# Kernel tuning notes

Hardware: AMD Instinct MI355X
Metric: run time of the kernel (lower is better)

## Reference

```python
import jax, jax.numpy as jnp
import numpy as np
from jax.ops import segment_sum

D = 64
NUM_REL = 500
NUM_NODES = 100000
NUM_EDGES = 2000000
BATCH = 8


def _mlp(x, W1, b1, W2, b2):
    # torch nn.Sequential(Linear, ReLU, Linear); W stored as [in, out]
    return jnp.maximum(x @ W1 + b1, 0.0) @ W2 + b2


def setup_inputs() -> dict:
    key = jax.random.key(0)
    ks = jax.random.split(key, 12)
    edge_index = jax.random.randint(ks[0], (2, NUM_EDGES), 0, NUM_NODES)
    edge_type = jax.random.randint(ks[1], (NUM_EDGES,), 0, NUM_REL)
    h_index = jax.random.randint(ks[2], (BATCH,), 0, NUM_NODES)
    relation_representations = jax.random.normal(ks[3], (NUM_REL, D), dtype=jnp.float32)
    s = 0.1
    params = dict(
        Wi1=jax.random.normal(ks[4], (2 * D, D), dtype=jnp.float32) * s,
        bi1=jnp.zeros((D,), jnp.float32),
        Wi2=jax.random.normal(ks[5], (D, D), dtype=jnp.float32) * s,
        bi2=jnp.zeros((D,), jnp.float32),
        Wc1=jax.random.normal(ks[6], (2 * D, D), dtype=jnp.float32) * s,
        bc1=jnp.zeros((D,), jnp.float32),
        Wc2=jax.random.normal(ks[7], (D, D), dtype=jnp.float32) * s,
        bc2=jnp.zeros((D,), jnp.float32),
        strength=jnp.asarray(0.1, jnp.float32),
    )
    return dict(edge_index=edge_index, edge_type=edge_type, h_index=h_index,
                relation_representations=relation_representations,
                num_nodes=NUM_NODES, **params)


def reference(edge_index, edge_type, h_index, relation_representations,
              num_nodes, Wi1, bi1, Wi2, bi2, Wc1, bc1, Wc2, bc2, strength):
    N = num_nodes
    rel_emb = relation_representations            # [R, D]
    rel_ctx = rel_emb.mean(axis=0)                # [D] global relation context
    src, dst = edge_index[0], edge_index[1]
    edge_rel = rel_emb[edge_type]                 # [E, D]
    not_self = (src != dst)                       # self-loop edge counted once per entity
    w_dst = not_self.astype(edge_rel.dtype)

    # per-node mean of incident-edge relation embeddings (valid_rels mean)
    feat_sum = segment_sum(edge_rel, src, num_segments=N) \
             + segment_sum(edge_rel * w_dst[:, None], dst, num_segments=N)   # [N, D]
    ones = jnp.ones_like(w_dst)
    cnt = segment_sum(ones, src, num_segments=N) \
        + segment_sum(w_dst, dst, num_segments=N)                            # [N]
    has_edge = cnt > 0
    avg = jnp.where(has_edge[:, None], feat_sum / jnp.maximum(cnt, 1.0)[:, None],
                    rel_ctx[None, :])             # [N, D] entity_relation_avg

    # nodes with at least one non-self neighbor
    nbr_cnt = segment_sum(w_dst, src, num_segments=N) \
            + segment_sum(w_dst, dst, num_segments=N)
    has_neighbor = nbr_cnt > 0

    ctx_b = jnp.broadcast_to(rel_ctx[None, :], avg.shape)
    interaction = _mlp(jnp.concatenate([avg, ctx_b], axis=-1), Wi1, bi1, Wi2, bi2)
    context = _mlp(jnp.concatenate([avg, avg], axis=-1), Wc1, bc1, Wc2, bc2)
    context_feat = jnp.where(has_neighbor[:, None], context, interaction)

    alpha = jnp.clip(strength, 0.0, 0.3)
    final = (1.0 - alpha) * avg + alpha * context_feat
    node_feat = jnp.where(has_edge[:, None], final, rel_ctx[None, :])        # [N, D]

    # relevant entities = query entities + 1-hop neighbors; others stay zero
    h_mask = jnp.zeros((N,), jnp.int32).at[h_index].set(1)
    nbr = jnp.zeros((N,), jnp.int32)
    nbr = nbr.at[dst].max(h_mask[src]).at[src].max(h_mask[dst])
    relevant = (h_mask + nbr) > 0                                            # [N]

    per_node = jnp.where(relevant[:, None], node_feat, 0.0)                  # [N, D]
    B = h_index.shape[0]
    return jnp.broadcast_to(per_node[None], (B, N, per_node.shape[-1]))      # [B, N, D]
```

## Files before the change

kernel.cpp:

```cpp
#include <hip/hip_runtime.h>

#define DD 64

typedef float f4v __attribute__((ext_vector_type(4)));

#define PACK(n, t, w) ((((unsigned)(n)) << 10) | (((unsigned)(t)) << 1) | (unsigned)(w))

__global__ __launch_bounds__(256) void k_fill0(float* __restrict__ out, size_t total4) {
    size_t i = (size_t)blockIdx.x * blockDim.x + threadIdx.x;
    const size_t stride = (size_t)gridDim.x * blockDim.x;
    f4v z = (f4v)(0.f);
    for (; i < total4; i += stride)
        __builtin_nontemporal_store(z, (f4v*)(out + i * 4));
}

__global__ void k_zero(unsigned* __restrict__ bitmap, int NB, int* __restrict__ counters) {
    int i = blockIdx.x * blockDim.x + threadIdx.x;
    if (i < NB) bitmap[i] = 0u;
    if (i < 2) counters[i] = 0;
}

__global__ __launch_bounds__(512) void k_ctx(const float* __restrict__ rel, int R,
                                             const int* __restrict__ h_index, int B,
                                             float* __restrict__ ctx,
                                             unsigned* __restrict__ bitmap) {
    __shared__ float part[8][DD];
    int lane = threadIdx.x & 63;
    int w = threadIdx.x >> 6;
    float s0 = 0.f, s1 = 0.f;
    int r = w;
    for (; r + 16 <= R; r += 16) {
        s0 += rel[(size_t)r * DD + lane];
        s1 += rel[(size_t)(r + 8) * DD + lane];
    }
    for (; r < R; r += 8) s0 += rel[(size_t)r * DD + lane];
    part[w][lane] = s0 + s1;
    __syncthreads();
    int t = threadIdx.x;
    if (t < DD) {
        float tot = 0.f;
#pragma unroll
        for (int i = 0; i < 8; ++i) tot += part[i][t];
        ctx[t] = tot / (float)R;
    }
    if (t < B) {
        int n = h_index[t];
        atomicOr(bitmap + ((unsigned)n >> 5), 1u << (n & 31));
    }
}

__device__ __forceinline__ bool is_q(int v, const int* hq) {
    bool m = false;
#pragma unroll
    for (int b = 0; b < 8; ++b) m |= (v == hq[b]);
    return m;
}

__global__ __launch_bounds__(256) void k_mark(const int* __restrict__ src,
                                              const int* __restrict__ dst,
                                              const int* __restrict__ h_index, int B,
                                              unsigned* __restrict__ bitmap, int E) {
    int hq[8];
#pragma unroll
    for (int b = 0; b < 8; ++b) hq[b] = (b < B) ? h_index[b] : -1;
    const int nth = gridDim.x * blockDim.x;
    const int tid = blockIdx.x * blockDim.x + threadIdx.x;
    const int E16 = E & ~15;
#define MARK1(sv, dv)                                                        \
    do {                                                                     \
        if (is_q(sv, hq)) atomicOr(bitmap + ((unsigned)(dv) >> 5), 1u << ((dv) & 31)); \
        if (is_q(dv, hq)) atomicOr(bitmap + ((unsigned)(sv) >> 5), 1u << ((sv) & 31)); \
    } while (0)
    for (int base = tid * 16; base < E16; base += nth * 16) {
        int4 s[4], d[4];
#pragma unroll
        for (int u = 0; u < 4; ++u) s[u] = *(const int4*)(src + base + u * 4);
#pragma unroll
        for (int u = 0; u < 4; ++u) d[u] = *(const int4*)(dst + base + u * 4);
#pragma unroll
        for (int u = 0; u < 4; ++u) {
            MARK1(s[u].x, d[u].x);
            MARK1(s[u].y, d[u].y);
            MARK1(s[u].z, d[u].z);
            MARK1(s[u].w, d[u].w);
        }
    }
    for (int e = E16 + tid; e < E; e += nth) MARK1(src[e], dst[e]);
#undef MARK1
}

__global__ __launch_bounds__(256) void k_compact(const unsigned* __restrict__ bitmap, int NB,
                                                 int* __restrict__ rel_list,
                                                 int* __restrict__ counters) {
    int i = blockIdx.x * blockDim.x + threadIdx.x;
    int lane = threadIdx.x & 63;
    unsigned word = (i < NB) ? bitmap[i] : 0u;
    int c = __popc(word);
    int incl = c;
#pragma unroll
    for (int sh = 1; sh < 64; sh <<= 1) {
        int t = __shfl_up(incl, sh);
        if (lane >= sh) incl += t;
    }
    int total = __shfl(incl, 63);
    if (total == 0) return;
    int b0 = 0;
    if (lane == 0) b0 = atomicAdd(counters + 0, total);
    b0 = __shfl(b0, 0);
    int off = b0 + incl - c;
    while (word) {
        int bit = __ffs(word) - 1;
        word &= word - 1;
        rel_list[off++] = i * 32 + bit;
    }
}

__global__ __launch_bounds__(256) void k_scan(const int* __restrict__ src,
                                              const int* __restrict__ dst,
                                              const int* __restrict__ etype,
                                              const unsigned* __restrict__ bitmap, int NB,
                                              unsigned* __restrict__ rlist,
                                              int* __restrict__ counters, int E) {
    extern __shared__ unsigned bm[];
    for (int i = threadIdx.x; i < NB; i += blockDim.x) bm[i] = bitmap[i];
    __syncthreads();
#define CHK(id) ((bm[(unsigned)(id) >> 5] >> ((unsigned)(id) & 31)) & 1u)
    const int lane = threadIdx.x & 63;
    const int wid = (blockIdx.x * blockDim.x + threadIdx.x) >> 6;
    const int nw = (gridDim.x * blockDim.x) >> 6;
    const int E16 = E & ~15;
    const int CH = 64 * 16;
    for (int cb = wid * CH; cb < E16; cb += nw * CH) {
        int base = cb + lane * 16;
        bool act = (base < E16);
        int4 s[4], d[4];
        if (act) {
#pragma unroll
            for (int u = 0; u < 4; ++u) s[u] = *(const int4*)(src + base + u * 4);
#pragma unroll
            for (int u = 0; u < 4; ++u) d[u] = *(const int4*)(dst + base + u * 4);
        }
        unsigned ms = 0u, md = 0u;
        if (act) {
#define TST(sv, dv, idx)                                        \
            do {                                                \
                unsigned bs = CHK(sv), bd = CHK(dv);            \
                unsigned neq = ((sv) != (dv)) ? 1u : 0u;        \
                ms |= bs << (idx);                              \
                md |= (bd & neq) << (idx);                      \
            } while (0)
#pragma unroll
            for (int u = 0; u < 4; ++u) {
                TST(s[u].x, d[u].x, u * 4 + 0);
                TST(s[u].y, d[u].y, u * 4 + 1);
                TST(s[u].z, d[u].z, u * 4 + 2);
                TST(s[u].w, d[u].w, u * 4 + 3);
            }
#undef TST
        }
        int c = __popc(ms) + __popc(md);
        int incl = c;
#pragma unroll
        for (int sh = 1; sh < 64; sh <<= 1) {
            int t = __shfl_up(incl, sh);
            if (lane >= sh) incl += t;
        }
        int total = __shfl(incl, 63);
        if (total == 0) continue;
        int b0 = 0;
        if (lane == 0) b0 = atomicAdd(counters + 1, total);
        b0 = __shfl(b0, 0);
        unsigned off = (unsigned)(b0 + incl - c);
        if (c) {
#define EMIT(sv, dv, idx)                                                     \
            do {                                                              \
                unsigned bit = 1u << (idx);                                   \
                if ((ms | md) & bit) {                                        \
                    int t = etype[base + (idx)];                              \
                    if (ms & bit) rlist[off++] = PACK(sv, t, ((sv) != (dv)) ? 1 : 0); \
                    if (md & bit) rlist[off++] = PACK(dv, t, 1);              \
                }                                                             \
            } while (0)
#pragma unroll
            for (int u = 0; u < 4; ++u) {
                EMIT(s[u].x, d[u].x, u * 4 + 0);
                EMIT(s[u].y, d[u].y, u * 4 + 1);
                EMIT(s[u].z, d[u].z, u * 4 + 2);
                EMIT(s[u].w, d[u].w, u * 4 + 3);
            }
#undef EMIT
        }
    }
    const int tid = blockIdx.x * blockDim.x + threadIdx.x;
    const int nth = gridDim.x * blockDim.x;
    for (int e = E16 + tid; e < E; e += nth) {
        int sv = src[e], dv = dst[e];
        unsigned bs = CHK(sv), bd = CHK(dv);
        unsigned neq = (sv != dv) ? 1u : 0u;
        int k = (int)bs + (int)(bd & neq);
        if (k == 0) continue;
        int t = etype[e];
        int o = atomicAdd(counters + 1, k);
        if (bs) rlist[o++] = PACK(sv, t, neq);
        if (bd & neq) rlist[o] = PACK(dv, t, 1);
    }
#undef CHK
}

__device__ __forceinline__ void proc_rec(unsigned rv, bool valid, int n,
                                         const float* __restrict__ rel, int lane,
                                         float& fs, int& cnt, int& nb) {
    bool want = valid && ((int)(rv >> 10) == n);
    unsigned long long mk = __ballot(want);
    while (mk) {
        int l = __ffsll(mk) - 1;
        mk &= mk - 1;
        unsigned v = __shfl(rv, l);
        int t = (int)((v >> 1) & 0x1FFu);
        fs += rel[t * DD + lane];
        cnt += 1;
        nb += (int)(v & 1u);
    }
}

__global__ __launch_bounds__(256) void k_gather(
    const int* __restrict__ rel_list, const int* __restrict__ counters,
    const unsigned* __restrict__ rlist,
    const float* __restrict__ rel, const float* __restrict__ ctx,
    const float* __restrict__ Wi1, const float* __restrict__ bi1,
    const float* __restrict__ Wi2, const float* __restrict__ bi2,
    const float* __restrict__ Wc1, const float* __restrict__ bc1,
    const float* __restrict__ Wc2, const float* __restrict__ bc2,
    const float* __restrict__ strength, float* __restrict__ out, int N, int B) {
    __shared__ float part[4][DD];
    __shared__ int pc[4], pn[4];
    int lane = threadIdx.x & 63;
    int wv = threadIdx.x >> 6;
    int C = counters[0];
    int M = counters[1];
    float alpha = fminf(fmaxf(strength[0], 0.f), 0.3f);
    float ctxj = ctx[lane];
    int nchunk = (M + 255) / 256;
    size_t plane = (size_t)N * DD;
    for (int i = blockIdx.x; i < C; i += gridDim.x) {
        int n = rel_list[i];
        float fs = 0.f;
        int cnt = 0, nb = 0;
        for (int ch = wv; ch < nchunk; ch += 4) {
            int bbase = ch * 256 + lane * 4;
            uint4 r = *(const uint4*)(rlist + bbase);
            proc_rec(r.x, bbase + 0 < M, n, rel, lane, fs, cnt, nb);
            proc_rec(r.y, bbase + 1 < M, n, rel, lane, fs, cnt, nb);
            proc_rec(r.z, bbase + 2 < M, n, rel, lane, fs, cnt, nb);
            proc_rec(r.w, bbase + 3 < M, n, rel, lane, fs, cnt, nb);
        }
        part[wv][lane] = fs;
        if (lane == 0) { pc[wv] = cnt; pn[wv] = nb; }
        __syncthreads();
        if (wv == 0) {
            fs = part[0][lane] + part[1][lane] + part[2][lane] + part[3][lane];
            cnt = pc[0] + pc[1] + pc[2] + pc[3];
            nb = pn[0] + pn[1] + pn[2] + pn[3];
            float res;
            if (cnt == 0) {
                res = ctxj;
            } else {
                float avg = fs / (float)cnt;
                bool hasnbr = (nb > 0);
                const float* W1 = hasnbr ? Wc1 : Wi1;
                const float* b1 = hasnbr ? bc1 : bi1;
                const float* W2 = hasnbr ? Wc2 : Wi2;
                const float* b2 = hasnbr ? bc2 : bi2;
                float h1 = b1[lane];
#pragma unroll 4
                for (int k = 0; k < DD; ++k) {
                    float a_k = __shfl(avg, k);
                    float x2 = hasnbr ? a_k : __shfl(ctxj, k);
                    h1 += a_k * W1[k * DD + lane] + x2 * W1[(DD + k) * DD + lane];
                }
                h1 = fmaxf(h1, 0.f);
                float o = b2[lane];
#pragma unroll 4
                for (int k = 0; k < DD; ++k)
                    o += __shfl(h1, k) * W2[k * DD + lane];
                res = (1.f - alpha) * avg + alpha * o;
            }
            float* p = out + (size_t)n * DD + lane;
            for (int b = 0; b < B; ++b) p[(size_t)b * plane] = res;
        }
        __syncthreads();
    }
}

extern "C" void kernel_launch(void* const* d_in, const int* in_sizes, int n_in,
                              void* d_out, int out_size, void* d_ws, size_t ws_size,
                              hipStream_t stream) {
    const int*   edge_index = (const int*)d_in[0];
    const int*   edge_type  = (const int*)d_in[1];
    const int*   h_index    = (const int*)d_in[2];
    const float* rel_emb    = (const float*)d_in[3];
    const float* Wi1 = (const float*)d_in[5];
    const float* bi1 = (const float*)d_in[6];
    const float* Wi2 = (const float*)d_in[7];
    const float* bi2 = (const float*)d_in[8];
    const float* Wc1 = (const float*)d_in[9];
    const float* bc1 = (const float*)d_in[10];
    const float* Wc2 = (const float*)d_in[11];
    const float* bc2 = (const float*)d_in[12];
    const float* strength = (const float*)d_in[13];
    float* out = (float*)d_out;

    const int E = in_sizes[1];
    const int B = in_sizes[2];
    const int R = in_sizes[3] / DD;
    const int N = out_size / (B * DD);
    const int NB = (N + 31) / 32;
    const int* src = edge_index;
    const int* dst = edge_index + E;

    char* w = (char*)d_ws;
    size_t off = 0;
    auto carve = [&](size_t bytes) -> char* {
        char* p = w + off;
        off += (bytes + 255) & ~(size_t)255;
        return p;
    };
    float*    ctx      = (float*)carve(DD * sizeof(float));
    int*      counters = (int*)carve(2 * sizeof(int));
    unsigned* bitmap   = (unsigned*)carve((size_t)NB * sizeof(unsigned));
    int*      rel_list = (int*)carve((size_t)N * sizeof(int));
    unsigned* rlist    = (unsigned*)carve(((size_t)2 * E + 512) * sizeof(unsigned));
    (void)ws_size; (void)n_in;

    const int BLK = 256;
    int gB = (NB + BLK - 1) / BLK;
    const int gE = 512;
    size_t total4 = (size_t)out_size / 4;

    hipLaunchKernelGGL(k_fill0, dim3(2048), dim3(BLK), 0, stream, out, total4);

    hipLaunchKernelGGL(k_zero, dim3(gB), dim3(BLK), 0, stream, bitmap, NB, counters);
    hipLaunchKernelGGL(k_ctx, dim3(1), dim3(512), 0, stream,
                       rel_emb, R, h_index, B, ctx, bitmap);
    hipLaunchKernelGGL(k_mark, dim3(gE), dim3(BLK), 0, stream,
                       src, dst, h_index, B, bitmap, E);
    hipLaunchKernelGGL(k_compact, dim3(gB), dim3(BLK), 0, stream,
                       bitmap, NB, rel_list, counters);
    hipLaunchKernelGGL(k_scan, dim3(gE), dim3(BLK), (size_t)NB * sizeof(unsigned), stream,
                       src, dst, edge_type, bitmap, NB, rlist, counters, E);
    hipLaunchKernelGGL(k_gather, dim3(512), dim3(BLK), 0, stream,
                       rel_list, counters, rlist, rel_emb, ctx,
                       Wi1, bi1, Wi2, bi2, Wc1, bc1, Wc2, bc2, strength, out, N, B);
}
```

Measured before the change: 109.6 us.

## Fuse zero/fill/compact kernels into mark and scan passes, raise grid size

Bitmap and counter zeroing are merged into the single-block context kernel. The output zero-fill is split in half and appended to the mark and scan kernels, and bitmap compaction is folded into the start of the scan kernel. The grid grows from 512 to 2048 blocks so the fused kernels cover all bitmap words. This cuts launches from seven to four and lets the large output fill overlap with the edge passes. In exchange, zeroing the bitmap with a single block is serial, and the compaction correctness now depends on the grid covering NB.

```diff
diff --git a/kernel.cpp b/kernel.cpp
--- a/kernel.cpp
+++ b/kernel.cpp
@@ -5,28 +5,18 @@
 typedef float f4v __attribute__((ext_vector_type(4)));
 
 #define PACK(n, t, w) ((((unsigned)(n)) << 10) | (((unsigned)(t)) << 1) | (unsigned)(w))
-
-__global__ __launch_bounds__(256) void k_fill0(float* __restrict__ out, size_t total4) {
-    size_t i = (size_t)blockIdx.x * blockDim.x + threadIdx.x;
-    const size_t stride = (size_t)gridDim.x * blockDim.x;
-    f4v z = (f4v)(0.f);
-    for (; i < total4; i += stride)
-        __builtin_nontemporal_store(z, (f4v*)(out + i * 4));
-}
-
-__global__ void k_zero(unsigned* __restrict__ bitmap, int NB, int* __restrict__ counters) {
-    int i = blockIdx.x * blockDim.x + threadIdx.x;
-    if (i < NB) bitmap[i] = 0u;
-    if (i < 2) counters[i] = 0;
-}
 
 __global__ __launch_bounds__(512) void k_ctx(const float* __restrict__ rel, int R,
                                              const int* __restrict__ h_index, int B,
                                              float* __restrict__ ctx,
-                                             unsigned* __restrict__ bitmap) {
+                                             unsigned* __restrict__ bitmap, int NB,
+                                             int* __restrict__ counters) {
     __shared__ float part[8][DD];
-    int lane = threadIdx.x & 63;
-    int w = threadIdx.x >> 6;
+    int t = threadIdx.x;
+    for (int i = t; i < NB; i += 512) bitmap[i] = 0u;
+    if (t < 2) counters[t] = 0;
+    int lane = t & 63;
+    int w = t >> 6;
     float s0 = 0.f, s1 = 0.f;
     int r = w;
     for (; r + 16 <= R; r += 16) {
@@ -36,7 +26,6 @@
     for (; r < R; r += 8) s0 += rel[(size_t)r * DD + lane];
     part[w][lane] = s0 + s1;
     __syncthreads();
-    int t = threadIdx.x;
     if (t < DD) {
         float tot = 0.f;
 #pragma unroll
@@ -56,10 +45,11 @@
     return m;
 }
 
-__global__ __launch_bounds__(256) void k_mark(const int* __restrict__ src,
-                                              const int* __restrict__ dst,
-                                              const int* __restrict__ h_index, int B,
-                                              unsigned* __restrict__ bitmap, int E) {
+__global__ __launch_bounds__(256) void k_markfill(const int* __restrict__ src,
+                                                  const int* __restrict__ dst,
+                                                  const int* __restrict__ h_index, int B,
+                                                  unsigned* __restrict__ bitmap, int E,
+                                                  float* __restrict__ out, size_t half4) {
     int hq[8];
 #pragma unroll
     for (int b = 0; b < 8; ++b) hq[b] = (b < B) ? h_index[b] : -1;
@@ -79,55 +69,58 @@
         for (int u = 0; u < 4; ++u) d[u] = *(const int4*)(dst + base + u * 4);
 #pragma unroll
         for (int u = 0; u < 4; ++u) {
-            MARK1(s[u].x, d[u].x);
-            MARK1(s[u].y, d[u].y);
-            MARK1(s[u].z, d[u].z);
-            MARK1(s[u].w, d[u].w);
+            MARK1(s[u].x, d[u].x); MARK1(s[u].y, d[u].y);
+            MARK1(s[u].z, d[u].z); MARK1(s[u].w, d[u].w);
         }
     }
     for (int e = E16 + tid; e < E; e += nth) MARK1(src[e], dst[e]);
 #undef MARK1
-}
-
-__global__ __launch_bounds__(256) void k_compact(const unsigned* __restrict__ bitmap, int NB,
-                                                 int* __restrict__ rel_list,
-                                                 int* __restrict__ counters) {
-    int i = blockIdx.x * blockDim.x + threadIdx.x;
-    int lane = threadIdx.x & 63;
-    unsigned word = (i < NB) ? bitmap[i] : 0u;
-    int c = __popc(word);
-    int incl = c;
-#pragma unroll
-    for (int sh = 1; sh < 64; sh <<= 1) {
-        int t = __shfl_up(incl, sh);
-        if (lane >= sh) incl += t;
-    }
-    int total = __shfl(incl, 63);
-    if (total == 0) return;
-    int b0 = 0;
-    if (lane == 0) b0 = atomicAdd(counters + 0, total);
-    b0 = __shfl(b0, 0);
-    int off = b0 + incl - c;
-    while (word) {
-        int bit = __ffs(word) - 1;
-        word &= word - 1;
-        rel_list[off++] = i * 32 + bit;
-    }
-}
-
-__global__ __launch_bounds__(256) void k_scan(const int* __restrict__ src,
-                                              const int* __restrict__ dst,
-                                              const int* __restrict__ etype,
-                                              const unsigned* __restrict__ bitmap, int NB,
-                                              unsigned* __restrict__ rlist,
-                                              int* __restrict__ counters, int E) {
+    f4v z = (f4v)(0.f);
+    for (size_t i = tid; i < half4; i += (size_t)nth)
+        __builtin_nontemporal_store(z, (f4v*)(out + i * 4));
+}
+
+__global__ __launch_bounds__(256) void k_scanfill(const int* __restrict__ src,
+                                                  const int* __restrict__ dst,
+                                                  const int* __restrict__ etype,
+                                                  const unsigned* __restrict__ bitmap, int NB,
+                                                  int* __restrict__ rel_list,
+                                                  unsigned* __restrict__ rlist,
+                                                  int* __restrict__ counters, int E,
+                                                  float* __restrict__ out,
+                                                  size_t half4, size_t total4) {
     extern __shared__ unsigned bm[];
+    const int lane = threadIdx.x & 63;
+    const int tid = blockIdx.x * blockDim.x + threadIdx.x;
+    const int nth = gridDim.x * blockDim.x;
+    {
+        int i = tid;
+        unsigned word = (i < NB) ? bitmap[i] : 0u;
+        int c = __popc(word);
+        int incl = c;
+#pragma unroll
+        for (int sh = 1; sh < 64; sh <<= 1) {
+            int t = __shfl_up(incl, sh);
+            if (lane >= sh) incl += t;
+        }
+        int total = __shfl(incl, 63);
+        if (total > 0) {
+            int b0 = 0;
+            if (lane == 0) b0 = atomicAdd(counters + 0, total);
+            b0 = __shfl(b0, 0);
+            int off = b0 + incl - c;
+            while (word) {
+                int bit = __ffs(word) - 1;
+                word &= word - 1;
+                rel_list[off++] = i * 32 + bit;
+            }
+        }
+    }
     for (int i = threadIdx.x; i < NB; i += blockDim.x) bm[i] = bitmap[i];
     __syncthreads();
 #define CHK(id) ((bm[(unsigned)(id) >> 5] >> ((unsigned)(id) & 31)) & 1u)
-    const int lane = threadIdx.x & 63;
-    const int wid = (blockIdx.x * blockDim.x + threadIdx.x) >> 6;
-    const int nw = (gridDim.x * blockDim.x) >> 6;
+    const int wid = tid >> 6;
+    const int nw = nth >> 6;
     const int E16 = E & ~15;
     const int CH = 64 * 16;
     for (int cb = wid * CH; cb < E16; cb += nw * CH) {
@@ -191,20 +184,22 @@
 #undef EMIT
         }
     }
-    const int tid = blockIdx.x * blockDim.x + threadIdx.x;
-    const int nth = gridDim.x * blockDim.x;
     for (int e = E16 + tid; e < E; e += nth) {
         int sv = src[e], dv = dst[e];
         unsigned bs = CHK(sv), bd = CHK(dv);
         unsigned neq = (sv != dv) ? 1u : 0u;
         int k = (int)bs + (int)(bd & neq);
-        if (k == 0) continue;
-        int t = etype[e];
-        int o = atomicAdd(counters + 1, k);
-        if (bs) rlist[o++] = PACK(sv, t, neq);
-        if (bd & neq) rlist[o] = PACK(dv, t, 1);
+        if (k) {
+            int t = etype[e];
+            int o = atomicAdd(counters + 1, k);
+            if (bs) rlist[o++] = PACK(sv, t, neq);
+            if (bd & neq) rlist[o] = PACK(dv, t, 1);
+        }
     }
 #undef CHK
+    f4v z = (f4v)(0.f);
+    for (size_t i = half4 + tid; i < total4; i += (size_t)nth)
+        __builtin_nontemporal_store(z, (f4v*)(out + i * 4));
 }
 
 __device__ __forceinline__ void proc_rec(unsigned rv, bool valid, int n,
@@ -333,21 +328,17 @@
     (void)ws_size; (void)n_in;
 
     const int BLK = 256;
-    int gB = (NB + BLK - 1) / BLK;
-    const int gE = 512;
+    const int gE = 2048;
     size_t total4 = (size_t)out_size / 4;
-
-    hipLaunchKernelGGL(k_fill0, dim3(2048), dim3(BLK), 0, stream, out, total4);
-
-    hipLaunchKernelGGL(k_zero, dim3(gB), dim3(BLK), 0, stream, bitmap, NB, counters);
+    size_t half4 = total4 / 2;
+
     hipLaunchKernelGGL(k_ctx, dim3(1), dim3(512), 0, stream,
-                       rel_emb, R, h_index, B, ctx, bitmap);
-    hipLaunchKernelGGL(k_mark, dim3(gE), dim3(BLK), 0, stream,
-                       src, dst, h_index, B, bitmap, E);
-    hipLaunchKernelGGL(k_compact, dim3(gB), dim3(BLK), 0, stream,
-                       bitmap, NB, rel_list, counters);
-    hipLaunchKernelGGL(k_scan, dim3(gE), dim3(BLK), (size_t)NB * sizeof(unsigned), stream,
-                       src, dst, edge_type, bitmap, NB, rlist, counters, E);
+                       rel_emb, R, h_index, B, ctx, bitmap, NB, counters);
+    hipLaunchKernelGGL(k_markfill, dim3(gE), dim3(BLK), 0, stream,
+                       src, dst, h_index, B, bitmap, E, out, half4);
+    hipLaunchKernelGGL(k_scanfill, dim3(gE), dim3(BLK), (size_t)NB * sizeof(unsigned), stream,
+                       src, dst, edge_type, bitmap, NB, rel_list, rlist, counters, E,
+                       out, half4, total4);
     hipLaunchKernelGGL(k_gather, dim3(512), dim3(BLK), 0, stream,
                        rel_list, counters, rlist, rel_emb, ctx,
                        Wi1, bi1, Wi2, bi2, Wc1, bc1, Wc2, bc2, strength, out, N, B);
```

Result: faster. 94.96 us (-13.3%).
